# Optimization experiments

Measured on AMD Instinct MI355X. Metric: run time of the kernel, lower is better.

The kernel has to match this reference:

```python
import jax, jax.numpy as jnp
import numpy as np

HIDDEN = 512
HEADS = 8
HEAD_DIM = HIDDEN // HEADS


def setup_inputs() -> dict:
    key = jax.random.key(0)
    ks = jax.random.split(key, 7)
    B, C, H, W = 8, HIDDEN, 32, 32
    scale = 1.0 / np.sqrt(C)
    inputs = jax.random.normal(ks[0], (B, C, H, W), dtype=jnp.float32)
    # 1x1 conv == per-pixel linear; store weights as [C_in, C_out]
    wq = jax.random.normal(ks[1], (C, HIDDEN), dtype=jnp.float32) * scale
    wk = jax.random.normal(ks[2], (C, HIDDEN), dtype=jnp.float32) * scale
    wv = jax.random.normal(ks[3], (C, HIDDEN), dtype=jnp.float32) * scale
    bq = jax.random.normal(ks[4], (HIDDEN,), dtype=jnp.float32) * 0.01
    bk = jax.random.normal(ks[5], (HIDDEN,), dtype=jnp.float32) * 0.01
    bv = jax.random.normal(ks[6], (HIDDEN,), dtype=jnp.float32) * 0.01
    return {"inputs": inputs, "wq": wq, "bq": bq, "wk": wk, "bk": bk, "wv": wv, "bv": bv}


def _proj_heads(x, w, b):
    # x: [B,C,H,W] -> tokens [B,heads,N,head_dim], matching transpose_for_scores
    B, C, H, W = x.shape
    t = jnp.einsum('bchw,cd->bhwd', x, w) + b          # [B,H,W,HIDDEN]
    t = t.reshape(B, H * W, HEADS, HEAD_DIM)
    return t.transpose(0, 2, 1, 3)                      # [B,heads,N,hd]


def reference(inputs, wq, bq, wk, bk, wv, bv):
    B, C, H, W = inputs.shape
    q = _proj_heads(inputs, wq, bq)
    k = _proj_heads(inputs, wk, bk)
    v = _proj_heads(inputs, wv, bv)
    # NOTE: original module applies NO 1/sqrt(d) scaling
    scores = jnp.einsum('bhnd,bhmd->bhnm', q, k)        # [B,heads,N,N]
    probs = jax.nn.softmax(scores, axis=-1)
    ctx = jnp.einsum('bhnm,bhmd->bhnd', probs, v)       # [B,heads,N,hd]
    # [B,heads,N,hd] -> [B,N,heads*hd] -> [B,H,W,C] -> [B,C,H,W]
    out = ctx.transpose(0, 2, 1, 3).reshape(B, H, W, HEADS * HEAD_DIM)
    return out.transpose(0, 3, 1, 2)
```

## Files before the change

kernel.cpp:

```cpp
#include <hip/hip_runtime.h>
#include <hip/hip_bf16.h>
#include <cmath>

#define B_     8
#define C_     512
#define N_     1024
#define HEADS_ 8
#define HD_    64
#define INST_  64

typedef short     v8s __attribute__((ext_vector_type(8)));
typedef _Float16  v8h __attribute__((ext_vector_type(8)));
typedef float    v16f __attribute__((ext_vector_type(16)));
typedef unsigned short ushort_t;
typedef unsigned int   uint_t;

__device__ inline ushort_t f2h(float x) {
    _Float16 h = (_Float16)x;
    ushort_t r; __builtin_memcpy(&r, &h, 2); return r;
}
__device__ inline uint_t pkbf(float a, float b) {
    __hip_bfloat162 p = __float22bfloat162_rn(make_float2(a, b));
    uint_t r; __builtin_memcpy(&r, &p, 4); return r;
}

__global__ __launch_bounds__(256) void prep_kernel(
    const float* __restrict__ wq, const float* __restrict__ wk,
    const float* __restrict__ wv,
    uint_t* __restrict__ wt)
{
    __shared__ uint_t LH[64 * 32];
    const int z = blockIdx.z;
    const float* src = (z == 0) ? wq : (z == 1) ? wk : wv;
    const size_t outRow0 = (size_t)z * 512 + blockIdx.x * 64;

    const int d0 = blockIdx.x * 64;
    const int c0 = blockIdx.y * 64;
    const int t  = threadIdx.x;

    #pragma unroll
    for (int rep = 0; rep < 2; ++rep) {
        int idx = rep * 256 + t;
        int cp  = idx >> 4;
        int dq  = idx & 15;
        float4 fa = *(const float4*)&src[(size_t)(c0 + 2 * cp) * 512 + d0 + dq * 4];
        float4 fb = *(const float4*)&src[(size_t)(c0 + 2 * cp + 1) * 512 + d0 + dq * 4];
        float aa[4] = {fa.x, fa.y, fa.z, fa.w};
        float bb[4] = {fb.x, fb.y, fb.z, fb.w};
        #pragma unroll
        for (int j = 0; j < 4; ++j) {
            int d_l = dq * 4 + j;
            LH[d_l * 32 + (cp ^ (d_l & 31))] =
                (uint_t)f2h(aa[j]) | ((uint_t)f2h(bb[j]) << 16);
        }
    }
    __syncthreads();

    const int d_l = t >> 2;
    const int wq4 = (t & 3) * 8;
    uint_t vh[8];
    #pragma unroll
    for (int i = 0; i < 8; ++i)
        vh[i] = LH[d_l * 32 + ((wq4 + i) ^ (d_l & 31))];
    size_t base = (outRow0 + d_l) * 256 + c0 / 2 + wq4;
    *(uint4*)&((uint_t*)wt)[base]     = *(uint4*)&vh[0];
    *(uint4*)&((uint_t*)wt)[base + 4] = *(uint4*)&vh[4];
}

__global__ __launch_bounds__(256) void proj_kernel(
    const float* __restrict__ x, const _Float16* __restrict__ wt,
    const float* __restrict__ bq, const float* __restrict__ bk,
    const float* __restrict__ bv,
    ushort_t* __restrict__ qf, ushort_t* __restrict__ kf,
    ushort_t* __restrict__ vt)
{
    __shared__ _Float16 POOL[12288];

    const int tok0  = blockIdx.x * 64;
    const int b     = tok0 >> 10;
    const int ntb   = tok0 & 1023;
    const int by    = blockIdx.y;
    const int which = by >> 2;
    const int nloc0 = (by & 3) * 128;

    const int t   = threadIdx.x;
    const int w   = t >> 6;
    const int l   = t & 63;
    const int l31 = l & 31;
    const int h5  = l >> 5;
    const int wm  = w & 1;
    const int wn  = w >> 1;

    const int g   = t & 3;
    const int r0  = t >> 2;
    const int sr0 = (r0 & 3) ^ ((r0 >> 2) & 3);
    const _Float16* baseB = wt + (size_t)(which * 512 + nloc0 + r0) * 512 + g * 8;

    const int cp = t & 15;
    const int tq = t >> 4;
    const float* baseX = x + (size_t)b * 524288 + (size_t)(2 * cp) * 1024
                       + ntb + 4 * tq;

    float4 paE0, paE1, paO0, paO1;
    v8h    pbE0, pbE1, pbO0, pbO1;

    auto loadE = [&](int s) {
        const float* px = baseX + (size_t)s * 32768;
        paE0 = *(const float4*)(px);
        paE1 = *(const float4*)(px + 1024);
        pbE0 = *(const v8h*)(baseB + s * 32);
        pbE1 = *(const v8h*)(baseB + 32768 + s * 32);
    };
    auto loadO = [&](int s) {
        const float* px = baseX + (size_t)s * 32768;
        paO0 = *(const float4*)(px);
        paO1 = *(const float4*)(px + 1024);
        pbO0 = *(const v8h*)(baseB + s * 32);
        pbO1 = *(const v8h*)(baseB + 32768 + s * 32);
    };
    auto storeE = [&](int off) {
        uint_t* Asu = (uint_t*)(POOL + off);
        float a0[4] = {paE0.x, paE0.y, paE0.z, paE0.w};
        float a1[4] = {paE1.x, paE1.y, paE1.z, paE1.w};
        #pragma unroll
        for (int i = 0; i < 4; ++i) {
            int rm  = 4 * tq + i;
            int srm = i ^ (tq & 3);
            Asu[rm * 16 + ((cp >> 2) ^ srm) * 4 + (cp & 3)] =
                (uint_t)f2h(a0[i]) | ((uint_t)f2h(a1[i]) << 16);
        }
        _Float16* Bs = POOL + off + 2048;
        *(v8h*)&Bs[(r0 * 4 + (g ^ sr0)) * 8] = pbE0;
        *(v8h*)&Bs[((64 + r0) * 4 + (g ^ sr0)) * 8] = pbE1;
    };
    auto storeO = [&](int off) {
        uint_t* Asu = (uint_t*)(POOL + off);
        float a0[4] = {paO0.x, paO0.y, paO0.z, paO0.w};
        float a1[4] = {paO1.x, paO1.y, paO1.z, paO1.w};
        #pragma unroll
        for (int i = 0; i < 4; ++i) {
            int rm  = 4 * tq + i;
            int srm = i ^ (tq & 3);
            Asu[rm * 16 + ((cp >> 2) ^ srm) * 4 + (cp & 3)] =
                (uint_t)f2h(a0[i]) | ((uint_t)f2h(a1[i]) << 16);
        }
        _Float16* Bs = POOL + off + 2048;
        *(v8h*)&Bs[(r0 * 4 + (g ^ sr0)) * 8] = pbO0;
        *(v8h*)&Bs[((64 + r0) * 4 + (g ^ sr0)) * 8] = pbO1;
    };

    v16f acc[2] = {{}, {}};

    auto compute = [&](int off) {
        #pragma unroll
        for (int kc = 0; kc < 2; ++kc) {
            int rm  = wm * 32 + l31;
            int srm = (rm & 3) ^ ((rm >> 2) & 3);
            v8h af = *(const v8h*)&POOL[off + (rm * 4 + ((kc * 2 + h5) ^ srm)) * 8];
            v8h bf[2];
            #pragma unroll
            for (int ns = 0; ns < 2; ++ns) {
                int rn  = wn * 64 + ns * 32 + l31;
                int srn = (rn & 3) ^ ((rn >> 2) & 3);
                bf[ns] = *(const v8h*)&POOL[off + 2048 +
                           (rn * 4 + ((kc * 2 + h5) ^ srn)) * 8];
            }
            #pragma unroll
            for (int ns = 0; ns < 2; ++ns)
                acc[ns] = __builtin_amdgcn_mfma_f32_32x32x16_f16(
                    af, bf[ns], acc[ns], 0, 0, 0);
        }
    };

    loadE(0);
    loadO(1);
    storeE(0);
    __syncthreads();

    for (int sp = 0; sp < 8; ++sp) {
        const int s = 2 * sp;
        if (s < 14) loadE(s + 2);
        compute(0);
        storeO(6144);
        __syncthreads();
        if (s < 13) loadO(s + 3);
        compute(6144);
        if (s < 14) {
            storeE(0);
            __syncthreads();
        }
    }

    __syncthreads();
    if (which < 2) {
        ushort_t* oh = (which == 0) ? qf : kf;
        const float* bias = (which == 0) ? bq : bk;
        const int head = (nloc0 + wn * 64) >> 6;
        float bvv[2];
        bvv[0] = bias[nloc0 + wn * 64 + l31];
        bvv[1] = bias[nloc0 + wn * 64 + 32 + l31];
        ushort_t* TWh = (ushort_t*)POOL + w * 2048;
        #pragma unroll
        for (int ns = 0; ns < 2; ++ns)
            #pragma unroll
            for (int r = 0; r < 16; ++r) {
                int tok = (r & 3) + 8 * (r >> 2) + 4 * h5;
                int hd  = ns * 32 + l31;
                int ch  = (hd >> 3) ^ (tok & 7);
                TWh[tok * 64 + ch * 8 + (hd & 7)] = f2h(acc[ns][r] + bvv[ns]);
            }
        __syncthreads();
        size_t baseg = (size_t)(b * HEADS_ + head) * 65536
                     + (size_t)(ntb + wm * 32) * 64;
        #pragma unroll
        for (int i = 0; i < 4; ++i) {
            int tok_r = i * 8 + (l >> 3);
            int ch_r  = l & 7;
            int ch_s  = ch_r ^ (tok_r & 7);
            uint4 v = *(uint4*)&TWh[tok_r * 64 + ch_s * 8];
            *(uint4*)&oh[baseg + (size_t)tok_r * 64 + ch_r * 8] = v;
        }
    } else {
        float bvv[2];
        #pragma unroll
        for (int ns = 0; ns < 2; ++ns)
            bvv[ns] = bv[nloc0 + wn * 64 + ns * 32 + l31];
        uint_t* TW = (uint_t*)POOL + w * 1024;
        #pragma unroll
        for (int ns = 0; ns < 2; ++ns)
            #pragma unroll
            for (int r = 0; r < 16; r += 2) {
                int tok_l = (r & 3) + 8 * (r >> 2) + 4 * h5;
                int hd_l  = ns * 32 + l31;
                TW[hd_l * 16 + ((tok_l >> 1) ^ (hd_l & 15))] =
                    pkbf(acc[ns][r] + bvv[ns], acc[ns][r + 1] + bvv[ns]);
            }
        __syncthreads();
        const int head = (nloc0 + wn * 64) >> 6;
        uint_t* vtu = (uint_t*)vt;
        size_t base = (size_t)(b * HEADS_ + head) * 32768 + (size_t)l * 512
                    + (ntb + wm * 32) / 2;
        #pragma unroll
        for (int c = 0; c < 4; ++c) {
            uint_t wd[4];
            #pragma unroll
            for (int kk = 0; kk < 4; ++kk) {
                int wsx = c * 4 + kk;
                int w3 = wsx & 7;
                int sw = (wsx & ~7) | (w3 & 1) | (((w3 >> 1) & 1) << 2)
                                   | (((w3 >> 2) & 1) << 1);
                wd[kk] = TW[l * 16 + (sw ^ (l & 15))];
            }
            *(uint4*)&vtu[base + c * 4] = *(uint4*)&wd[0];
        }
    }
}

__global__ __launch_bounds__(256) void attn_kernel(
    const ushort_t* __restrict__ qf, const ushort_t* __restrict__ kf,
    const ushort_t* __restrict__ vt, float* __restrict__ out)
{
    __shared__ _Float16 POOL[16640];
    _Float16* KH = POOL;
    ushort_t* VT = (ushort_t*)(POOL + 8192);
    float*    RS = (float*)(POOL + 16384);

    const int inst  = blockIdx.x;
    const int chunk = blockIdx.y;
    const int t     = threadIdx.x;
    const int w     = t >> 6;
    const int l     = t & 63;
    const int l31   = l & 31;
    const int h5    = l >> 5;

    const ushort_t* Qf = qf + (size_t)inst * 65536;
    const ushort_t* Kf = kf + (size_t)inst * 65536;
    const ushort_t* Vt = vt + (size_t)inst * 65536;

    const int qbase = chunk * 128 + w * 32;

    v8h aq[4];
    #pragma unroll
    for (int ks = 0; ks < 4; ++ks)
        aq[ks] = *(const v8h*)&Qf[(size_t)(qbase + l31) * 64 + ks * 16 + h5 * 8];

    const int g   = t & 7;
    const int r0  = t >> 3;
    const int swz = g ^ (r0 & 7);
    const ushort_t* baseK = Kf + (size_t)r0 * 64 + g * 8;
    const ushort_t* baseV = Vt + (size_t)r0 * 1024 + g * 8;

    v8h pkE0, pkE1, pkO0, pkO1;
    v8s pvE0, pvE1, pvO0, pvO1;

    auto loadE = [&](int kt) {
        pkE0 = *(const v8h*)(baseK + (size_t)kt * 4096);
        pkE1 = *(const v8h*)(baseK + (size_t)kt * 4096 + 2048);
        pvE0 = *(const v8s*)(baseV + (size_t)kt * 64);
        pvE1 = *(const v8s*)(baseV + 32768 + (size_t)kt * 64);
    };
    auto loadO = [&](int kt) {
        pkO0 = *(const v8h*)(baseK + (size_t)kt * 4096);
        pkO1 = *(const v8h*)(baseK + (size_t)kt * 4096 + 2048);
        pvO0 = *(const v8s*)(baseV + (size_t)kt * 64);
        pvO1 = *(const v8s*)(baseV + 32768 + (size_t)kt * 64);
    };
    auto storeE = [&](int off) {
        int so0 = (r0 * 8 + swz) * 8;
        int so1 = ((32 + r0) * 8 + swz) * 8;
        *(v8h*)&KH[off + so0] = pkE0;
        *(v8h*)&KH[off + so1] = pkE1;
        *(v8s*)&VT[off + so0] = pvE0;
        *(v8s*)&VT[off + so1] = pvE1;
    };
    auto storeO = [&](int off) {
        int so0 = (r0 * 8 + swz) * 8;
        int so1 = ((32 + r0) * 8 + swz) * 8;
        *(v8h*)&KH[off + so0] = pkO0;
        *(v8h*)&KH[off + so1] = pkO1;
        *(v8s*)&VT[off + so0] = pvO0;
        *(v8s*)&VT[off + so1] = pvO1;
    };

    v16f O0 = {}, O1 = {};
    float rsumv = 0.f;

    auto compute = [&](int off) {
        #pragma unroll
        for (int t2 = 0; t2 < 2; ++t2) {
            v16f s = {};
            int kvrow = t2 * 32 + l31;
            #pragma unroll
            for (int ks = 0; ks < 4; ++ks) {
                int so = (kvrow * 8 + ((ks * 2 + h5) ^ (kvrow & 7))) * 8;
                v8h khf = *(const v8h*)&KH[off + so];
                s = __builtin_amdgcn_mfma_f32_32x32x16_f16(khf, aq[ks], s, 0, 0, 0);
            }
            float e0[8], e1[8];
            #pragma unroll
            for (int j = 0; j < 8; ++j) {
                e0[j] = __expf(s[j] - 64.0f);
                e1[j] = __expf(s[8 + j] - 64.0f);
                rsumv += e0[j] + e1[j];
            }
            uint4 u0, u1;
            u0.x = pkbf(e0[0], e0[1]); u0.y = pkbf(e0[2], e0[3]);
            u0.z = pkbf(e0[4], e0[5]); u0.w = pkbf(e0[6], e0[7]);
            u1.x = pkbf(e1[0], e1[1]); u1.y = pkbf(e1[2], e1[3]);
            u1.z = pkbf(e1[4], e1[5]); u1.w = pkbf(e1[6], e1[7]);
            v8s p0 = __builtin_bit_cast(v8s, u0);
            v8s p1 = __builtin_bit_cast(v8s, u1);

            #pragma unroll
            for (int hh = 0; hh < 2; ++hh) {
                int rv = hh * 32 + l31;
                int g0 = (4 * t2 + h5)     ^ (rv & 7);
                int g1 = (4 * t2 + 2 + h5) ^ (rv & 7);
                v8s bv0 = *(const v8s*)&VT[off + (rv * 8 + g0) * 8];
                v8s bv1 = *(const v8s*)&VT[off + (rv * 8 + g1) * 8];
                if (hh == 0) {
                    O0 = __builtin_amdgcn_mfma_f32_32x32x16_bf16(p0, bv0, O0, 0, 0, 0);
                    O0 = __builtin_amdgcn_mfma_f32_32x32x16_bf16(p1, bv1, O0, 0, 0, 0);
                } else {
                    O1 = __builtin_amdgcn_mfma_f32_32x32x16_bf16(p0, bv0, O1, 0, 0, 0);
                    O1 = __builtin_amdgcn_mfma_f32_32x32x16_bf16(p1, bv1, O1, 0, 0, 0);
                }
            }
        }
    };

    loadE(0);
    loadO(1);
    storeE(0);
    __syncthreads();

    for (int sp = 0; sp < 8; ++sp) {
        const int kt = 2 * sp;
        if (kt < 14) loadE(kt + 2);
        compute(0);
        storeO(4096);
        __syncthreads();
        if (kt < 13) loadO(kt + 3);
        compute(4096);
        if (kt < 14) {
            storeE(0);
            __syncthreads();
        }
    }

    float tot = rsumv + __shfl_xor(rsumv, 32, 64);
    if (h5 == 0) RS[w * 32 + l31] = 1.0f / tot;
    __syncthreads();
    float invr[16];
    #pragma unroll
    for (int r = 0; r < 16; ++r)
        invr[r] = RS[w * 32 + (r & 3) + 8 * (r >> 2) + 4 * h5];

    float* TWf = (float*)(POOL + w * 4096);
    #pragma unroll
    for (int hh = 0; hh < 2; ++hh) {
        const v16f& O = hh ? O1 : O0;
        int c_loc = hh * 32 + l31;
        #pragma unroll
        for (int qd = 0; qd < 4; ++qd) {
            int gs = (2 * qd + h5) ^ (l31 & 7);
            float4 o4;
            o4.x = O[qd * 4 + 0] * invr[qd * 4 + 0];
            o4.y = O[qd * 4 + 1] * invr[qd * 4 + 1];
            o4.z = O[qd * 4 + 2] * invr[qd * 4 + 2];
            o4.w = O[qd * 4 + 3] * invr[qd * 4 + 3];
            *(float4*)&TWf[c_loc * 32 + gs * 4] = o4;
        }
    }
    __syncthreads();

    const int b    = inst >> 3;
    const int head = inst & 7;
    float* ob = out + (size_t)b * C_ * N_;
    #pragma unroll
    for (int i = 0; i < 8; ++i) {
        int c_r = i * 8 + (l >> 3);
        int gq  = l & 7;
        int gs  = gq ^ (c_r & 7);
        float4 v = *(const float4*)&TWf[c_r * 32 + gs * 4];
        *(float4*)&ob[(size_t)(head * 64 + c_r) * N_ + qbase + gq * 4] = v;
    }
}

extern "C" void kernel_launch(void* const* d_in, const int* in_sizes, int n_in,
                              void* d_out, int out_size, void* d_ws, size_t ws_size,
                              hipStream_t stream) {
    const float* x  = (const float*)d_in[0];
    const float* wq = (const float*)d_in[1];
    const float* bq = (const float*)d_in[2];
    const float* wk = (const float*)d_in[3];
    const float* bk = (const float*)d_in[4];
    const float* wv = (const float*)d_in[5];
    const float* bv = (const float*)d_in[6];
    float* out = (float*)d_out;

    char* ws = (char*)d_ws;
    _Float16* wt = (_Float16*)(ws);
    ushort_t* qf = (ushort_t*)(ws + 9961472);
    ushort_t* kf = (ushort_t*)(ws + 18350080);
    ushort_t* vt = (ushort_t*)(ws + 26738688);

    prep_kernel<<<dim3(8, 8, 3), 256, 0, stream>>>(wq, wk, wv, (uint_t*)wt);
    proj_kernel<<<dim3(128, 12), 256, 0, stream>>>(x, wt, bq, bk, bv,
                                                   qf, kf, vt);
    attn_kernel<<<dim3(64, 8), 256, 0, stream>>>(qf, kf, vt, out);
}
```

Baseline: 140.0 us.

## Stage weight and K/V tiles via direct global-to-LDS async loads

In both the projection and attention kernels, weight and K/V tiles are now copied straight into shared memory with global_load_lds (16-byte per lane). This replaces the old path that loaded into registers and then wrote to LDS. The XOR swizzle is moved to the global address side so each wave writes a contiguous LDS block. The unrolled even/odd double-buffer loop becomes a single 16-step loop that prefetches one step ahead. This is meant to free VGPRs and remove LDS store instructions, but the prefetch distance is now shorter and correctness relies on the barrier waiting for the outstanding async loads.

```diff
diff --git a/kernel.cpp b/kernel.cpp
--- a/kernel.cpp
+++ b/kernel.cpp
@@ -14,6 +14,9 @@
 typedef float    v16f __attribute__((ext_vector_type(16)));
 typedef unsigned short ushort_t;
 typedef unsigned int   uint_t;
+
+typedef const __attribute__((address_space(1))) unsigned int gu32_t;
+typedef __attribute__((address_space(3)))       unsigned int lu32_t;
 
 __device__ inline ushort_t f2h(float x) {
     _Float16 h = (_Float16)x;
@@ -90,35 +93,38 @@
     const int h5  = l >> 5;
     const int wm  = w & 1;
     const int wn  = w >> 1;
-
-    const int g   = t & 3;
-    const int r0  = t >> 2;
-    const int sr0 = (r0 & 3) ^ ((r0 >> 2) & 3);
-    const _Float16* baseB = wt + (size_t)(which * 512 + nloc0 + r0) * 512 + g * 8;
+    const int wrow = which * 512 + nloc0;
 
     const int cp = t & 15;
     const int tq = t >> 4;
     const float* baseX = x + (size_t)b * 524288 + (size_t)(2 * cp) * 1024
                        + ntb + 4 * tq;
 
+    auto stageB = [&](int off, int step) {
+        #pragma unroll
+        for (int j = 0; j < 2; ++j) {
+            int s  = j * 256 + t;
+            int rn = s >> 2;
+            int gg = (s & 3) ^ ((rn & 3) ^ ((rn >> 2) & 3));
+            const _Float16* gB = wt + (size_t)(wrow + rn) * 512 + step * 32 + gg * 8;
+            int lbase = off + 2048 + (j * 256 + (t & 192)) * 8;
+            __builtin_amdgcn_global_load_lds((gu32_t*)gB, (lu32_t*)&POOL[lbase],
+                                             16, 0, 0);
+        }
+    };
+
     float4 paE0, paE1, paO0, paO1;
-    v8h    pbE0, pbE1, pbO0, pbO1;
-
     auto loadE = [&](int s) {
         const float* px = baseX + (size_t)s * 32768;
         paE0 = *(const float4*)(px);
         paE1 = *(const float4*)(px + 1024);
-        pbE0 = *(const v8h*)(baseB + s * 32);
-        pbE1 = *(const v8h*)(baseB + 32768 + s * 32);
     };
     auto loadO = [&](int s) {
         const float* px = baseX + (size_t)s * 32768;
         paO0 = *(const float4*)(px);
         paO1 = *(const float4*)(px + 1024);
-        pbO0 = *(const v8h*)(baseB + s * 32);
-        pbO1 = *(const v8h*)(baseB + 32768 + s * 32);
-    };
-    auto storeE = [&](int off) {
+    };
+    auto storeAE = [&](int off) {
         uint_t* Asu = (uint_t*)(POOL + off);
         float a0[4] = {paE0.x, paE0.y, paE0.z, paE0.w};
         float a1[4] = {paE1.x, paE1.y, paE1.z, paE1.w};
@@ -129,11 +135,8 @@
             Asu[rm * 16 + ((cp >> 2) ^ srm) * 4 + (cp & 3)] =
                 (uint_t)f2h(a0[i]) | ((uint_t)f2h(a1[i]) << 16);
         }
-        _Float16* Bs = POOL + off + 2048;
-        *(v8h*)&Bs[(r0 * 4 + (g ^ sr0)) * 8] = pbE0;
-        *(v8h*)&Bs[((64 + r0) * 4 + (g ^ sr0)) * 8] = pbE1;
-    };
-    auto storeO = [&](int off) {
+    };
+    auto storeAO = [&](int off) {
         uint_t* Asu = (uint_t*)(POOL + off);
         float a0[4] = {paO0.x, paO0.y, paO0.z, paO0.w};
         float a1[4] = {paO1.x, paO1.y, paO1.z, paO1.w};
@@ -144,9 +147,6 @@
             Asu[rm * 16 + ((cp >> 2) ^ srm) * 4 + (cp & 3)] =
                 (uint_t)f2h(a0[i]) | ((uint_t)f2h(a1[i]) << 16);
         }
-        _Float16* Bs = POOL + off + 2048;
-        *(v8h*)&Bs[(r0 * 4 + (g ^ sr0)) * 8] = pbO0;
-        *(v8h*)&Bs[((64 + r0) * 4 + (g ^ sr0)) * 8] = pbO1;
     };
 
     v16f acc[2] = {{}, {}};
@@ -173,22 +173,25 @@
     };
 
     loadE(0);
+    stageB(0, 0);
     loadO(1);
-    storeE(0);
-    __syncthreads();
-
-    for (int sp = 0; sp < 8; ++sp) {
-        const int s = 2 * sp;
-        if (s < 14) loadE(s + 2);
-        compute(0);
-        storeO(6144);
+    storeAE(0);
+    __syncthreads();
+
+    for (int step = 0; step < 16; ++step) {
+        const int off  = (step & 1) ? 6144 : 0;
+        const int offn = (step & 1) ? 0 : 6144;
+        if (step < 15) stageB(offn, step + 1);
+        if (step < 14) {
+            if ((step & 1) == 0) loadE(step + 2);
+            else                 loadO(step + 2);
+        }
+        compute(off);
+        if (step < 15) {
+            if ((step & 1) == 0) storeAO(offn);
+            else                 storeAE(offn);
+        }
         __syncthreads();
-        if (s < 13) loadO(s + 3);
-        compute(6144);
-        if (s < 14) {
-            storeE(0);
-            __syncthreads();
-        }
     }
 
     __syncthreads();
@@ -284,42 +287,20 @@
     for (int ks = 0; ks < 4; ++ks)
         aq[ks] = *(const v8h*)&Qf[(size_t)(qbase + l31) * 64 + ks * 16 + h5 * 8];
 
-    const int g   = t & 7;
-    const int r0  = t >> 3;
-    const int swz = g ^ (r0 & 7);
-    const ushort_t* baseK = Kf + (size_t)r0 * 64 + g * 8;
-    const ushort_t* baseV = Vt + (size_t)r0 * 1024 + g * 8;
-
-    v8h pkE0, pkE1, pkO0, pkO1;
-    v8s pvE0, pvE1, pvO0, pvO1;
-
-    auto loadE = [&](int kt) {
-        pkE0 = *(const v8h*)(baseK + (size_t)kt * 4096);
-        pkE1 = *(const v8h*)(baseK + (size_t)kt * 4096 + 2048);
-        pvE0 = *(const v8s*)(baseV + (size_t)kt * 64);
-        pvE1 = *(const v8s*)(baseV + 32768 + (size_t)kt * 64);
-    };
-    auto loadO = [&](int kt) {
-        pkO0 = *(const v8h*)(baseK + (size_t)kt * 4096);
-        pkO1 = *(const v8h*)(baseK + (size_t)kt * 4096 + 2048);
-        pvO0 = *(const v8s*)(baseV + (size_t)kt * 64);
-        pvO1 = *(const v8s*)(baseV + 32768 + (size_t)kt * 64);
-    };
-    auto storeE = [&](int off) {
-        int so0 = (r0 * 8 + swz) * 8;
-        int so1 = ((32 + r0) * 8 + swz) * 8;
-        *(v8h*)&KH[off + so0] = pkE0;
-        *(v8h*)&KH[off + so1] = pkE1;
-        *(v8s*)&VT[off + so0] = pvE0;
-        *(v8s*)&VT[off + so1] = pvE1;
-    };
-    auto storeO = [&](int off) {
-        int so0 = (r0 * 8 + swz) * 8;
-        int so1 = ((32 + r0) * 8 + swz) * 8;
-        *(v8h*)&KH[off + so0] = pkO0;
-        *(v8h*)&KH[off + so1] = pkO1;
-        *(v8s*)&VT[off + so0] = pvO0;
-        *(v8s*)&VT[off + so1] = pvO1;
+    auto stage = [&](int off, int kt) {
+        #pragma unroll
+        for (int j = 0; j < 2; ++j) {
+            int s   = j * 256 + t;
+            int rho = s >> 3;
+            int gg  = (s & 7) ^ (rho & 7);
+            const ushort_t* gK = Kf + (size_t)kt * 4096 + rho * 64 + gg * 8;
+            const ushort_t* gV = Vt + (size_t)kt * 64 + (size_t)rho * 1024 + gg * 8;
+            int lbase = off + (j * 256 + (t & 192)) * 8;
+            __builtin_amdgcn_global_load_lds((gu32_t*)gK, (lu32_t*)&KH[lbase],
+                                             16, 0, 0);
+            __builtin_amdgcn_global_load_lds((gu32_t*)gV, (lu32_t*)&VT[lbase],
+                                             16, 0, 0);
+        }
     };
 
     v16f O0 = {}, O1 = {};
@@ -369,23 +350,15 @@
         }
     };
 
-    loadE(0);
-    loadO(1);
-    storeE(0);
-    __syncthreads();
-
-    for (int sp = 0; sp < 8; ++sp) {
-        const int kt = 2 * sp;
-        if (kt < 14) loadE(kt + 2);
-        compute(0);
-        storeO(4096);
+    stage(0, 0);
+    __syncthreads();
+
+    for (int kt = 0; kt < 16; ++kt) {
+        const int off  = (kt & 1) ? 4096 : 0;
+        const int offn = (kt & 1) ? 0 : 4096;
+        if (kt < 15) stage(offn, kt + 1);
+        compute(off);
         __syncthreads();
-        if (kt < 13) loadO(kt + 3);
-        compute(4096);
-        if (kt < 14) {
-            storeE(0);
-            __syncthreads();
-        }
     }
 
     float tot = rsumv + __shfl_xor(rsumv, 32, 64);
```

After: 146.1 us. +4.3%, slower.
